# Optimization experiments

Measured on AMD Instinct MI355X. Metric: run time of the kernel, lower is better.

## Reference

```python
import jax, jax.numpy as jnp
import numpy as np

TEMPERATURE = 0.6


def setup_inputs() -> dict:
    key = jax.random.key(0)
    k1, k2, k3 = jax.random.split(key, 3)
    B, IN, OUT, C = 8192, 256, 32, 50
    x = jax.random.uniform(k1, (B, IN), dtype=jnp.float32)
    weight = jax.random.normal(k2, (C, OUT, IN), dtype=jnp.float32) * 0.05
    bias = jax.random.normal(k3, (C, 1, OUT), dtype=jnp.float32) * 0.05
    return {"x": x, "weight": weight, "bias": bias}


def reference(x, weight, bias):
    # gamma[c,i] = L1 norm of weight over out dim: sum_o |W[c,o,i]|
    gamma = jnp.sum(jnp.abs(weight), axis=1)            # [C, IN]
    alpha = jax.nn.softmax(gamma / TEMPERATURE, axis=1)  # [C, IN]
    alpha_norm = alpha / jnp.max(alpha, axis=1, keepdims=True)  # [C, IN]
    # gated input per class: [C, B, IN]
    xg = x[None, :, :] * alpha_norm[:, None, :]
    # per-class GEMM: y[c,b,o] = sum_i xg[c,b,i] * W[c,o,i]
    y = jnp.einsum('cbi,coi->cbo', xg, weight) + bias    # [C, B, OUT]
    return jnp.transpose(y, (1, 0, 2))                   # [B, C, OUT]
```

## Files before the change

### kernel.cpp

```cpp
#include <hip/hip_runtime.h>
#include <hip/hip_bf16.h>

typedef __bf16 bf16x8 __attribute__((ext_vector_type(8)));
typedef float  f32x4  __attribute__((ext_vector_type(4)));

#define B_ROWS 8192
#define IN_DIM 256
#define OUT_DIM 32
#define NCLS 50
#define INV_T (1.0f / 0.6f)

#define CVT_BLOCKS 1024
#define ROWTILES 16
#define NCHUNK 8

__device__ __forceinline__ void gload_lds16(const void* g, void* l) {
    __builtin_amdgcn_global_load_lds(
        (const __attribute__((address_space(1))) void*)g,
        (__attribute__((address_space(3))) void*)l, 16, 0, 0);
}

__global__ __launch_bounds__(256) void prep(const float* __restrict__ x,
                                            const float* __restrict__ w,
                                            __bf16* __restrict__ xb,
                                            __bf16* __restrict__ wb) {
    __shared__ float wm[4];
    int bid = blockIdx.x;
    if (bid < NCLS) {
        int c = bid;
        int i = threadIdx.x;
        const float* wc = w + (size_t)c * OUT_DIM * IN_DIM + i;
        float wv[OUT_DIM];
#pragma unroll
        for (int o = 0; o < OUT_DIM; ++o) wv[o] = wc[o * IN_DIM];
        float gsum = 0.f;
#pragma unroll
        for (int o = 0; o < OUT_DIM; ++o) gsum += fabsf(wv[o]);
        float m = gsum;
#pragma unroll
        for (int s = 1; s < 64; s <<= 1) m = fmaxf(m, __shfl_xor(m, s));
        if ((threadIdx.x & 63) == 0) wm[threadIdx.x >> 6] = m;
        __syncthreads();
        m = fmaxf(fmaxf(wm[0], wm[1]), fmaxf(wm[2], wm[3]));
        float an = __expf((gsum - m) * INV_T);
        __bf16* wo = wb + (size_t)c * OUT_DIM * IN_DIM + i;
#pragma unroll
        for (int o = 0; o < OUT_DIM; ++o)
            wo[o * IN_DIM] = (__bf16)(wv[o] * an);
    } else {
        int i = ((bid - NCLS) * 256 + threadIdx.x) * 8;
        float4 v0 = *reinterpret_cast<const float4*>(x + i);
        float4 v1 = *reinterpret_cast<const float4*>(x + i + 4);
        bf16x8 r;
        r[0] = (__bf16)v0.x; r[1] = (__bf16)v0.y; r[2] = (__bf16)v0.z; r[3] = (__bf16)v0.w;
        r[4] = (__bf16)v1.x; r[5] = (__bf16)v1.y; r[6] = (__bf16)v1.z; r[7] = (__bf16)v1.w;
        *reinterpret_cast<bf16x8*>(xb + i) = r;
    }
}

__global__ __launch_bounds__(256, 2) void gemm(const __bf16* __restrict__ xb,
                                               const __bf16* __restrict__ wb,
                                               const float* __restrict__ bias,
                                               float* __restrict__ out) {
    __shared__ __align__(16) char lds[4 * 2 * 8192];

    int bid = blockIdx.x;
    int cp = bid >> 4;
    int rt = bid & (ROWTILES - 1);
    int c0 = cp * 2;
    int row0 = rt * 512;
    int lane = threadIdx.x & 63;
    int w4 = threadIdx.x >> 6;
    int l15 = lane & 15;
    int g = lane >> 4;
    int s31 = lane & 31;
    int lr = lane >> 5;

    char* Abuf0 = lds + w4 * 16384;
    char* Abuf1 = Abuf0 + 8192;

    const char* arows = (const char*)(xb + (size_t)(row0 + w4 * 128) * IN_DIM);
#define STAGE_A(BUF, CHUNK)                                                       \
    _Pragma("unroll") for (int il = 0; il < 8; ++il) {                            \
        int r = (CHUNK) * 16 + 2 * il + lr;                                       \
        gload_lds16(arows + (size_t)r * 512 + ((s31 ^ (r & 15)) * 16),            \
                    (BUF) + il * 1024);                                           \
    }
    STAGE_A(Abuf0, 0)

    const char* wsrc = (const char*)(wb + (size_t)c0 * OUT_DIM * IN_DIM);
#pragma unroll
    for (int jw = 0; jw < 8; ++jw) {
        int re = jw * 8 + w4 * 2;
        int r = re + lr;
        gload_lds16(wsrc + (size_t)r * 512 + ((s31 ^ (r & 15)) * 16),
                    lds + (re >> 4) * 16384 + 8192 + (re & 15) * 512);
    }

    asm volatile("s_waitcnt vmcnt(0)" ::: "memory");
    __syncthreads();
    __builtin_amdgcn_sched_barrier(0);

    bf16x8 W[2][16];
#pragma unroll
    for (int ci = 0; ci < 2; ++ci)
#pragma unroll
        for (int kk = 0; kk < 8; ++kk) {
            int slot = (4 * kk + g) ^ l15;
            W[ci][kk]     = *reinterpret_cast<const bf16x8*>(
                lds + (2 * ci) * 16384 + 8192 + l15 * 512 + slot * 16);
            W[ci][8 + kk] = *reinterpret_cast<const bf16x8*>(
                lds + (2 * ci + 1) * 16384 + 8192 + l15 * 512 + slot * 16);
        }
#pragma unroll
    for (int ci = 0; ci < 2; ++ci)
#pragma unroll
        for (int kk = 0; kk < 16; ++kk)
            asm volatile("" : "+v"(W[ci][kk]));
    __builtin_amdgcn_sched_barrier(0);
    __syncthreads();

    f32x4 bv00 = *reinterpret_cast<const f32x4*>(bias + c0 * OUT_DIM + g * 4);
    f32x4 bv01 = *reinterpret_cast<const f32x4*>(bias + c0 * OUT_DIM + 16 + g * 4);
    f32x4 bv10 = *reinterpret_cast<const f32x4*>(bias + (c0 + 1) * OUT_DIM + g * 4);
    f32x4 bv11 = *reinterpret_cast<const f32x4*>(bias + (c0 + 1) * OUT_DIM + 16 + g * 4);

    float* orow = out + (size_t)(row0 + w4 * 128 + l15) * (NCLS * OUT_DIM) + c0 * OUT_DIM + g * 4;

#pragma unroll
    for (int k = 0; k < NCHUNK; ++k) {
        char* cur = (k & 1) ? Abuf1 : Abuf0;
        char* nxt = (k & 1) ? Abuf0 : Abuf1;
        if (k + 1 < NCHUNK) {
            STAGE_A(nxt, k + 1)
            asm volatile("s_waitcnt vmcnt(12)" ::: "memory");
        } else {
            asm volatile("s_waitcnt vmcnt(4)" ::: "memory");
        }
        __builtin_amdgcn_sched_barrier(0);

        f32x4 acc00 = bv00;
        f32x4 acc01 = bv01;
        f32x4 acc10 = bv10;
        f32x4 acc11 = bv11;
#pragma unroll
        for (int kk = 0; kk < 8; ++kk) {
            int slot = (4 * kk + g) ^ l15;
            bf16x8 a = *reinterpret_cast<const bf16x8*>(cur + (size_t)l15 * 512 + slot * 16);
            acc00 = __builtin_amdgcn_mfma_f32_16x16x32_bf16(W[0][kk],     a, acc00, 0, 0, 0);
            acc01 = __builtin_amdgcn_mfma_f32_16x16x32_bf16(W[0][8 + kk], a, acc01, 0, 0, 0);
            acc10 = __builtin_amdgcn_mfma_f32_16x16x32_bf16(W[1][kk],     a, acc10, 0, 0, 0);
            acc11 = __builtin_amdgcn_mfma_f32_16x16x32_bf16(W[1][8 + kk], a, acc11, 0, 0, 0);
        }
        float* op = orow + (size_t)k * 16 * (NCLS * OUT_DIM);
        *reinterpret_cast<f32x4*>(op) = acc00;
        *reinterpret_cast<f32x4*>(op + 16) = acc01;
        *reinterpret_cast<f32x4*>(op + OUT_DIM) = acc10;
        *reinterpret_cast<f32x4*>(op + OUT_DIM + 16) = acc11;
    }
#undef STAGE_A
}

extern "C" void kernel_launch(void* const* d_in, const int* in_sizes, int n_in,
                              void* d_out, int out_size, void* d_ws, size_t ws_size,
                              hipStream_t stream) {
    const float* x    = (const float*)d_in[0];
    const float* w    = (const float*)d_in[1];
    const float* bias = (const float*)d_in[2];
    float* out = (float*)d_out;

    __bf16* xb = (__bf16*)d_ws;
    __bf16* wb = xb + (size_t)B_ROWS * IN_DIM;

    prep<<<NCLS + CVT_BLOCKS, 256, 0, stream>>>(x, w, xb, wb);
    gemm<<<25 * ROWTILES, 256, 0, stream>>>(xb, wb, bias, out);
}
```

Before: 28.25 us.

## Split A staging into K-half subchunks with four-deep prefetch ring

Changes A-tile staging from double-buffered 16-row full-K chunks to a four-slot ring of half-K subchunks (16 rows x 128 K), prefetched three ahead with hand-tuned vmcnt waits. The weight tile is repacked into a flat LDS layout overlapping the ring, and the bias loads are moved before the initial barrier. The aim is deeper memory-level parallelism and better overlap of global loads with MFMA work. The cost is more complex wait-count bookkeeping, which could be fragile if the counts are wrong.

```diff
diff --git a/kernel.cpp b/kernel.cpp
--- a/kernel.cpp
+++ b/kernel.cpp
@@ -12,7 +12,7 @@
 
 #define CVT_BLOCKS 1024
 #define ROWTILES 16
-#define NCHUNK 8
+#define NSUB 16
 
 __device__ __forceinline__ void gload_lds16(const void* g, void* l) {
     __builtin_amdgcn_global_load_lds(
@@ -62,7 +62,7 @@
                                                const __bf16* __restrict__ wb,
                                                const float* __restrict__ bias,
                                                float* __restrict__ out) {
-    __shared__ __align__(16) char lds[4 * 2 * 8192];
+    __shared__ __align__(16) char lds[4 * 4 * 4096];
 
     int bid = blockIdx.x;
     int cp = bid >> 4;
@@ -75,18 +75,10 @@
     int g = lane >> 4;
     int s31 = lane & 31;
     int lr = lane >> 5;
+    int row4 = lane >> 4;
+    int p15 = lane & 15;
 
-    char* Abuf0 = lds + w4 * 16384;
-    char* Abuf1 = Abuf0 + 8192;
-
-    const char* arows = (const char*)(xb + (size_t)(row0 + w4 * 128) * IN_DIM);
-#define STAGE_A(BUF, CHUNK)                                                       \
-    _Pragma("unroll") for (int il = 0; il < 8; ++il) {                            \
-        int r = (CHUNK) * 16 + 2 * il + lr;                                       \
-        gload_lds16(arows + (size_t)r * 512 + ((s31 ^ (r & 15)) * 16),            \
-                    (BUF) + il * 1024);                                           \
-    }
-    STAGE_A(Abuf0, 0)
+    char* wavelds = lds + w4 * 16384;
 
     const char* wsrc = (const char*)(wb + (size_t)c0 * OUT_DIM * IN_DIM);
 #pragma unroll
@@ -94,8 +86,12 @@
         int re = jw * 8 + w4 * 2;
         int r = re + lr;
         gload_lds16(wsrc + (size_t)r * 512 + ((s31 ^ (r & 15)) * 16),
-                    lds + (re >> 4) * 16384 + 8192 + (re & 15) * 512);
+                    lds + re * 512);
     }
+    f32x4 bv00 = *reinterpret_cast<const f32x4*>(bias + c0 * OUT_DIM + g * 4);
+    f32x4 bv01 = *reinterpret_cast<const f32x4*>(bias + c0 * OUT_DIM + 16 + g * 4);
+    f32x4 bv10 = *reinterpret_cast<const f32x4*>(bias + (c0 + 1) * OUT_DIM + g * 4);
+    f32x4 bv11 = *reinterpret_cast<const f32x4*>(bias + (c0 + 1) * OUT_DIM + 16 + g * 4);
 
     asm volatile("s_waitcnt vmcnt(0)" ::: "memory");
     __syncthreads();
@@ -106,59 +102,72 @@
     for (int ci = 0; ci < 2; ++ci)
 #pragma unroll
         for (int kk = 0; kk < 8; ++kk) {
-            int slot = (4 * kk + g) ^ l15;
+            int wr1 = ci * 32 + l15;
+            int wr2 = wr1 + 16;
             W[ci][kk]     = *reinterpret_cast<const bf16x8*>(
-                lds + (2 * ci) * 16384 + 8192 + l15 * 512 + slot * 16);
+                lds + (size_t)wr1 * 512 + (((4 * kk + g) ^ l15) * 16));
             W[ci][8 + kk] = *reinterpret_cast<const bf16x8*>(
-                lds + (2 * ci + 1) * 16384 + 8192 + l15 * 512 + slot * 16);
+                lds + (size_t)wr2 * 512 + (((4 * kk + g) ^ l15) * 16));
         }
 #pragma unroll
     for (int ci = 0; ci < 2; ++ci)
 #pragma unroll
         for (int kk = 0; kk < 16; ++kk)
             asm volatile("" : "+v"(W[ci][kk]));
+    asm volatile("" : "+v"(bv00), "+v"(bv01), "+v"(bv10), "+v"(bv11));
     __builtin_amdgcn_sched_barrier(0);
     __syncthreads();
 
-    f32x4 bv00 = *reinterpret_cast<const f32x4*>(bias + c0 * OUT_DIM + g * 4);
-    f32x4 bv01 = *reinterpret_cast<const f32x4*>(bias + c0 * OUT_DIM + 16 + g * 4);
-    f32x4 bv10 = *reinterpret_cast<const f32x4*>(bias + (c0 + 1) * OUT_DIM + g * 4);
-    f32x4 bv11 = *reinterpret_cast<const f32x4*>(bias + (c0 + 1) * OUT_DIM + 16 + g * 4);
-
+    const char* arows = (const char*)(xb + (size_t)(row0 + w4 * 128) * IN_DIM);
     float* orow = out + (size_t)(row0 + w4 * 128 + l15) * (NCLS * OUT_DIM) + c0 * OUT_DIM + g * 4;
 
+#define STAGE_SC(SC)                                                               \
+    _Pragma("unroll") for (int j = 0; j < 4; ++j) {                                \
+        int rl = j * 4 + row4;                                                     \
+        gload_lds16(arows + (size_t)((SC) >> 1) * 8192 + ((SC) & 1) * 256          \
+                        + (size_t)rl * 512 + ((p15 ^ rl) * 16),                    \
+                    wavelds + ((SC) & 3) * 4096 + j * 1024);                       \
+    }
+#define VMW(N) asm volatile("s_waitcnt vmcnt(" #N ")" ::: "memory")
+
+    STAGE_SC(0)
+    STAGE_SC(1)
+    STAGE_SC(2)
+
+    f32x4 acc00, acc01, acc10, acc11;
+
 #pragma unroll
-    for (int k = 0; k < NCHUNK; ++k) {
-        char* cur = (k & 1) ? Abuf1 : Abuf0;
-        char* nxt = (k & 1) ? Abuf0 : Abuf1;
-        if (k + 1 < NCHUNK) {
-            STAGE_A(nxt, k + 1)
-            asm volatile("s_waitcnt vmcnt(12)" ::: "memory");
-        } else {
-            asm volatile("s_waitcnt vmcnt(4)" ::: "memory");
-        }
+    for (int sc = 0; sc < NSUB; ++sc) {
+        if (sc <= 12) STAGE_SC(sc + 3)
+        if (sc <= 1)       VMW(12);
+        else if (sc == 2)  VMW(16);
+        else if (sc <= 12) { if (sc & 1) VMW(16); else VMW(20); }
+        else if (sc <= 14) VMW(12);
+        else               VMW(4);
         __builtin_amdgcn_sched_barrier(0);
 
-        f32x4 acc00 = bv00;
-        f32x4 acc01 = bv01;
-        f32x4 acc10 = bv10;
-        f32x4 acc11 = bv11;
+        if (!(sc & 1)) { acc00 = bv00; acc01 = bv01; acc10 = bv10; acc11 = bv11; }
+        char* buf = wavelds + (sc & 3) * 4096;
+        int h4 = (sc & 1) * 4;
 #pragma unroll
-        for (int kk = 0; kk < 8; ++kk) {
-            int slot = (4 * kk + g) ^ l15;
-            bf16x8 a = *reinterpret_cast<const bf16x8*>(cur + (size_t)l15 * 512 + slot * 16);
-            acc00 = __builtin_amdgcn_mfma_f32_16x16x32_bf16(W[0][kk],     a, acc00, 0, 0, 0);
-            acc01 = __builtin_amdgcn_mfma_f32_16x16x32_bf16(W[0][8 + kk], a, acc01, 0, 0, 0);
-            acc10 = __builtin_amdgcn_mfma_f32_16x16x32_bf16(W[1][kk],     a, acc10, 0, 0, 0);
-            acc11 = __builtin_amdgcn_mfma_f32_16x16x32_bf16(W[1][8 + kk], a, acc11, 0, 0, 0);
+        for (int kkl = 0; kkl < 4; ++kkl) {
+            bf16x8 a = *reinterpret_cast<const bf16x8*>(
+                buf + (size_t)l15 * 256 + (((4 * kkl + g) ^ l15) * 16));
+            acc00 = __builtin_amdgcn_mfma_f32_16x16x32_bf16(W[0][h4 + kkl],     a, acc00, 0, 0, 0);
+            acc01 = __builtin_amdgcn_mfma_f32_16x16x32_bf16(W[0][8 + h4 + kkl], a, acc01, 0, 0, 0);
+            acc10 = __builtin_amdgcn_mfma_f32_16x16x32_bf16(W[1][h4 + kkl],     a, acc10, 0, 0, 0);
+            acc11 = __builtin_amdgcn_mfma_f32_16x16x32_bf16(W[1][8 + h4 + kkl], a, acc11, 0, 0, 0);
         }
-        float* op = orow + (size_t)k * 16 * (NCLS * OUT_DIM);
-        *reinterpret_cast<f32x4*>(op) = acc00;
-        *reinterpret_cast<f32x4*>(op + 16) = acc01;
-        *reinterpret_cast<f32x4*>(op + OUT_DIM) = acc10;
-        *reinterpret_cast<f32x4*>(op + OUT_DIM + 16) = acc11;
+        if (sc & 1) {
+            float* op = orow + (size_t)(sc >> 1) * 16 * (NCLS * OUT_DIM);
+            *reinterpret_cast<f32x4*>(op) = acc00;
+            *reinterpret_cast<f32x4*>(op + 16) = acc01;
+            *reinterpret_cast<f32x4*>(op + OUT_DIM) = acc10;
+            *reinterpret_cast<f32x4*>(op + OUT_DIM + 16) = acc11;
+        }
     }
-#undef STAGE_A
+#undef STAGE_SC
+#undef VMW
 }
 
 extern "C" void kernel_launch(void* const* d_in, const int* in_sizes, int n_in,
```

Measured after the change: 28.71 us. No clear change (+1.6%).
